# Performance work log

Measured on AMD Instinct MI355X. Metric: run time of the kernel, lower is better.

Reference implementation:

```python
import jax, jax.numpy as jnp
import numpy as np
from jax import lax

NPOINT = 1024
NSAMPLE = 32
RADIUS = 0.6
BN_EPS = 1e-5


def square_distance(src, dst):
    # src (B,S,3), dst (B,N,3) -> (B,S,N) squared distances
    d = -2.0 * jnp.einsum('bsc,bnc->bsn', src, dst)
    d = d + jnp.sum(src ** 2, -1)[:, :, None]
    d = d + jnp.sum(dst ** 2, -1)[:, None, :]
    return d


def farthest_point_sample(xyz, npoint):
    B, N, _ = xyz.shape
    bidx = jnp.arange(B)

    def step(carry, _):
        distance, farthest = carry
        centroid = xyz[bidx, farthest]                      # (B,3)
        dist = jnp.sum((xyz - centroid[:, None, :]) ** 2, -1)  # (B,N)
        distance = jnp.minimum(distance, dist)
        new_far = jnp.argmax(distance, -1)
        return (distance, new_far), farthest

    init = (jnp.full((B, N), 1e10, xyz.dtype), jnp.zeros((B,), jnp.int32))
    _, idxs = lax.scan(step, init, None, length=npoint)
    return idxs.T                                            # (B,npoint)


def ball_query(xyz, new_xyz, radius, nsample):
    B, N, _ = xyz.shape
    sqr = square_distance(new_xyz, xyz)                      # (B,S,N)
    idx = jnp.where(sqr <= radius ** 2, jnp.arange(N)[None, None, :], N)
    idx = jnp.sort(idx, axis=-1)[:, :, :nsample]             # (B,S,K)
    first = idx[:, :, :1]
    return jnp.where(idx == N, first, idx)


def gather2(points, idx):
    # points (B,N,C), idx (B,S) -> (B,S,C)
    return jax.vmap(lambda p, i: p[i])(points, idx)


def gather3(points, idx):
    # points (B,N,C), idx (B,S,K) -> (B,S,K,C)
    return jax.vmap(lambda p, i: p[i])(points, idx)


def sa_forward(xyz, features, params):
    fps_idx = lax.stop_gradient(farthest_point_sample(xyz, NPOINT))
    new_xyz = gather2(xyz, fps_idx)                          # (B,S,3)
    idx = lax.stop_gradient(ball_query(xyz, new_xyz, RADIUS, NSAMPLE))
    grouped_xyz = gather3(xyz, idx) - new_xyz[:, :, None, :] # (B,S,K,3)
    grouped_feat = gather3(features.transpose(0, 2, 1), idx) # (B,S,K,C)
    g = jnp.concatenate([grouped_xyz, grouped_feat], -1)     # (B,S,K,C+3)
    g = g.transpose(0, 3, 2, 1)                              # (B,Cin,K,S)
    for w, b, ga, be in params:
        g = jnp.einsum('oc,bcks->boks', w, g) + b[None, :, None, None]
        mu = jnp.mean(g, axis=(0, 2, 3), keepdims=True)
        var = jnp.var(g, axis=(0, 2, 3), keepdims=True)
        g = ga[None, :, None, None] * (g - mu) * lax.rsqrt(var + BN_EPS) \
            + be[None, :, None, None]
        g = jax.nn.relu(g)
    new_features = jnp.max(g, axis=2)                        # (B,Cout,S)
    return new_xyz, new_features


def setup_inputs() -> dict:
    key = jax.random.key(0)
    ks = jax.random.split(key, 8)
    B, N, C = 16, 4096, 128
    cin = C + 3
    mlp = [128, 128, 256]
    inp = {
        'xyz': jax.random.normal(ks[0], (B, N, 3), jnp.float32),
        'features': jax.random.normal(ks[1], (B, C, N), jnp.float32),
    }
    prev = cin
    for i, out in enumerate(mlp):
        inp[f'w{i}'] = jax.random.normal(ks[2 + i], (out, prev), jnp.float32) * 0.05
        inp[f'b{i}'] = jnp.zeros((out,), jnp.float32)
        inp[f'gamma{i}'] = jnp.ones((out,), jnp.float32)
        inp[f'beta{i}'] = jnp.zeros((out,), jnp.float32)
        prev = out
    return inp


def reference(xyz, features, w0, b0, gamma0, beta0, w1, b1, gamma1, beta1,
              w2, b2, gamma2, beta2):
    params = [(w0, b0, gamma0, beta0), (w1, b1, gamma1, beta1),
              (w2, b2, gamma2, beta2)]
    return sa_forward(xyz, features, params)
```

## Files before the change

kernel.cpp:

```cpp
#include <hip/hip_runtime.h>

#define B_ 16
#define N_ 4096
#define S_ 1024
#define K_ 32
#define PITCH2 136
#define PITCH1 168

typedef unsigned long long u64;
typedef short bf16x8 __attribute__((ext_vector_type(8)));
typedef unsigned short u16x8 __attribute__((ext_vector_type(8)));
typedef float f32x4 __attribute__((ext_vector_type(4)));
typedef float f32x2 __attribute__((ext_vector_type(2)));

__device__ __forceinline__ unsigned short f2bf(float f) {
  unsigned u = __float_as_uint(f);
  unsigned r = (u + 0x7FFFu + ((u >> 16) & 1u)) >> 16;
  return (unsigned short)r;
}
__device__ __forceinline__ float bf2f(unsigned short h) {
  return __uint_as_float(((unsigned)h) << 16);
}

#define DPP_MAX(v, ctrl)                                                        \
  {                                                                             \
    int _t = __builtin_amdgcn_update_dpp(__float_as_int(v), __float_as_int(v),  \
                                         ctrl, 0xf, 0xf, false);                \
    v = fmaxf(v, __int_as_float(_t));                                           \
  }

__global__ __launch_bounds__(512) void k_front(
    const float* __restrict__ xyz, float* __restrict__ new_xyz,
    const float* __restrict__ feat, unsigned short* __restrict__ featT,
    const float* __restrict__ w0, const float* __restrict__ w1,
    const float* __restrict__ w2, unsigned short* __restrict__ wbf0,
    unsigned short* __restrict__ wbf1, unsigned short* __restrict__ wbf2,
    float* __restrict__ stats) {
  __shared__ __align__(16) float smem[N_ * 4 + S_ + 64];
  int blk = blockIdx.x, t = threadIdx.x;

  if (blk < 16) {
#pragma clang fp contract(off)
#if __has_builtin(__builtin_amdgcn_s_setprio)
    __builtin_amdgcn_s_setprio(3);
#endif
    float4* pts = (float4*)smem;
    int* idxs = (int*)(smem + N_ * 4);
    u64* swk = (u64*)(smem + N_ * 4 + S_);
    int b = blk;
    const float* base = xyz + (size_t)b * N_ * 3;
    for (int i = t; i < N_; i += 512)
      pts[i] = make_float4(base[i * 3], base[i * 3 + 1], base[i * 3 + 2], 0.0f);
    if (t == 0) idxs[0] = 0;
    __syncthreads();
    f32x2 px[4], py[4], pz[4], pd[4];
    int i0 = t * 8;
    #pragma unroll
    for (int j = 0; j < 4; ++j) {
      float4 p0 = pts[i0 + 2 * j], p1 = pts[i0 + 2 * j + 1];
      px[j] = (f32x2){p0.x, p1.x};
      py[j] = (f32x2){p0.y, p1.y};
      pz[j] = (f32x2){p0.z, p1.z};
      pd[j] = (f32x2){1e10f, 1e10f};
    }
    int cur = 0;
    for (int it = 0; it < S_; ++it) {
      float4 c = pts[cur];
      f32x2 c2x = (f32x2){c.x, c.x}, c2y = (f32x2){c.y, c.y}, c2z = (f32x2){c.z, c.z};
      float bestv = -1.0f; int besti = 0;
      #pragma unroll
      for (int j = 0; j < 4; ++j) {
        f32x2 dx = px[j] - c2x;
        f32x2 dy = py[j] - c2y;
        f32x2 dz = pz[j] - c2z;
        f32x2 d = (dx * dx + dy * dy) + dz * dz;
        f32x2 dm = __builtin_elementwise_min(pd[j], d);
        pd[j] = dm;
        if (dm.x > bestv) { bestv = dm.x; besti = 2 * j; }
        if (dm.y > bestv) { bestv = dm.y; besti = 2 * j + 1; }
      }
      float v = bestv;
      DPP_MAX(v, 0x111);
      DPP_MAX(v, 0x112);
      DPP_MAX(v, 0x114);
      DPP_MAX(v, 0x118);
      DPP_MAX(v, 0x142);
      DPP_MAX(v, 0x143);
      float wmax = __int_as_float(__builtin_amdgcn_readlane(__float_as_int(v), 63));
      u64 mask = __ballot(bestv == wmax);
      int owner = __ffsll((long long)mask) - 1;
      int widx = __builtin_amdgcn_readlane(i0 + besti, owner);
      if ((t & 63) == 0)
        swk[(it & 1) * 8 + (t >> 6)] =
            ((u64)__float_as_uint(wmax) << 32) | (unsigned)(4095 - widx);
      __syncthreads();
      const u64* kk = swk + (it & 1) * 8;
      u64 k0 = kk[0];
      #pragma unroll
      for (int w = 1; w < 8; ++w) if (kk[w] > k0) k0 = kk[w];
      cur = 4095 - (int)(unsigned)(k0 & 0xFFFFFFFFull);
      if (t == 0 && it + 1 < S_) idxs[it + 1] = cur;
    }
    __syncthreads();
    for (int i = t; i < S_; i += 512) {
      float4 v = pts[idxs[i]];
      size_t o = ((size_t)b * S_ + i) * 3;
      new_xyz[o] = v.x; new_xyz[o + 1] = v.y; new_xyz[o + 2] = v.z;
    }
  } else if (blk < 32) {
    int id = (blk - 16) * 512 + t;
    const int st = 16 * 512;
    for (int i = id; i < 32768; i += st) stats[i] = 0.0f;
    for (int i = id; i < 128 * 160; i += st) {
      int n = i / 160, k = i - n * 160;
      float v = (k < 128) ? w0[n * 131 + 3 + k] : (k < 131) ? w0[n * 131 + k - 128] : 0.0f;
      wbf0[i] = f2bf(v);
    }
    for (int i = id; i < 128 * 128; i += st) wbf1[i] = f2bf(w1[i]);
    for (int i = id; i < 256 * 128; i += st) wbf2[i] = f2bf(w2[i]);
  } else {
    float (*tile)[33] = (float(*)[33])smem;
    int blk2 = blk - 32;
    int n0 = (blk2 & 127) * 32;
    int c0 = ((blk2 >> 7) & 3) * 32;
    int b = blk2 >> 9;
    int tx = t & 31, ty = t >> 5;
    #pragma unroll
    for (int j = 0; j < 32; j += 16)
      tile[ty + j][tx] = feat[((size_t)b * 128 + c0 + ty + j) * N_ + n0 + tx];
    __syncthreads();
    #pragma unroll
    for (int j = 0; j < 32; j += 16)
      featT[((size_t)b * N_ + n0 + ty + j) * 128 + c0 + tx] = f2bf(tile[tx][ty + j]);
  }
}

__global__ __launch_bounds__(256) void k_ballq(const float* __restrict__ xyz,
                                               const float* __restrict__ new_xyz,
                                               int* __restrict__ ball_idx) {
  int b = blockIdx.y;
  int s = blockIdx.x * 4 + (threadIdx.x >> 6);
  int lane = threadIdx.x & 63;
  const float* pb = xyz + (size_t)b * N_ * 3;
  size_t q = (size_t)b * S_ + s;
  float qx = new_xyz[q * 3], qy = new_xyz[q * 3 + 1], qz = new_xyz[q * 3 + 2];
  float sq = __fadd_rn(__fadd_rn(__fmul_rn(qx, qx), __fmul_rn(qy, qy)), __fmul_rn(qz, qz));
  int* out = ball_idx + q * K_;
  int total = 0;
  int first_idx = -1;
  for (int basei = 0; basei < N_; basei += 64) {
    int i = basei + lane;
    float fx = pb[i * 3], fy = pb[i * 3 + 1], fz = pb[i * 3 + 2];
    float dot = __fmul_rn(qx, fx);
    dot = __fadd_rn(dot, __fmul_rn(qy, fy));
    dot = __fadd_rn(dot, __fmul_rn(qz, fz));
    float sd = __fadd_rn(__fadd_rn(__fmul_rn(fx, fx), __fmul_rn(fy, fy)), __fmul_rn(fz, fz));
    float dist = __fadd_rn(__fadd_rn(__fmul_rn(-2.0f, dot), sq), sd);
    bool within = (dist <= 0.36f);
    u64 m = __ballot(within);
    if (first_idx < 0 && m) first_idx = basei + __ffsll((long long)m) - 1;
    if (within) {
      int pos = total + __popcll(m & ((1ull << lane) - 1ull));
      if (pos < K_) out[pos] = i;
    }
    total += (int)__popcll(m);
    if (total >= K_) break;
  }
  if (total < K_) {
    int k2 = total + lane;
    if (k2 < K_) out[k2] = first_idx;
  }
}

#define MFMA(a, b, c) __builtin_amdgcn_mfma_f32_16x16x32_bf16(a, b, c, 0, 0, 0)
#define NTILES 4096

__global__ __launch_bounds__(256) void k_layer1(
    const float* __restrict__ xyz, const float* __restrict__ new_xyz,
    const unsigned short* __restrict__ featT, const int* __restrict__ ball_idx,
    const unsigned short* __restrict__ wbf0, const float* __restrict__ b0,
    unsigned short* __restrict__ y, float* __restrict__ stats) {
  __shared__ __align__(16) unsigned short Wl[128 * PITCH1];
  __shared__ float sbias[128];
  int t = threadIdx.x;
  int w = t >> 6, L = t & 63, lm = L & 15, lg = L >> 4;
  {
    int n = t >> 1, h = t & 1;
    const uint4* wr = (const uint4*)(wbf0 + n * 160 + h * 80);
    uint4* wl = (uint4*)(Wl + n * PITCH1 + h * 80);
    #pragma unroll
    for (int i = 0; i < 10; ++i) wl[i] = wr[i];
    if (t < 128) sbias[t] = b0[t];
  }
  __syncthreads();

  for (int tile = blockIdx.x; tile < NTILES; tile += gridDim.x) {
    int bb = tile >> 8;
    int s0 = (tile & 255) * 4;
    size_t qg = (size_t)bb * S_ + s0 + w;

    int p0 = ball_idx[qg * K_ + lm];
    int p1 = ball_idx[qg * K_ + 16 + lm];
    const unsigned short* f0 = featT + ((size_t)bb * N_ + p0) * 128;
    const unsigned short* f1 = featT + ((size_t)bb * N_ + p1) * 128;
    bf16x8 a0[5], a1[5];
    #pragma unroll
    for (int kt = 0; kt < 4; ++kt) {
      a0[kt] = *(const bf16x8*)(f0 + kt * 32 + lg * 8);
      a1[kt] = *(const bf16x8*)(f1 + kt * 32 + lg * 8);
    }
    a0[4] = (bf16x8){0, 0, 0, 0, 0, 0, 0, 0};
    a1[4] = (bf16x8){0, 0, 0, 0, 0, 0, 0, 0};
    if (lg == 0) {
      float nx = new_xyz[qg * 3], ny = new_xyz[qg * 3 + 1], nz = new_xyz[qg * 3 + 2];
      const float* pp0 = xyz + ((size_t)bb * N_ + p0) * 3;
      const float* pp1 = xyz + ((size_t)bb * N_ + p1) * 3;
      a0[4][0] = (short)f2bf(pp0[0] - nx);
      a0[4][1] = (short)f2bf(pp0[1] - ny);
      a0[4][2] = (short)f2bf(pp0[2] - nz);
      a1[4][0] = (short)f2bf(pp1[0] - nx);
      a1[4][1] = (short)f2bf(pp1[1] - ny);
      a1[4][2] = (short)f2bf(pp1[2] - nz);
    }
    f32x4 acc[2][8];
    #pragma unroll
    for (int mi = 0; mi < 2; ++mi)
      #pragma unroll
      for (int nt = 0; nt < 8; ++nt) acc[mi][nt] = (f32x4){0.f, 0.f, 0.f, 0.f};
    #pragma unroll
    for (int kt = 0; kt < 5; ++kt) {
      int ko = kt * 32 + lg * 8;
      bf16x8 bv[8];
      #pragma unroll
      for (int nt = 0; nt < 8; ++nt)
        bv[nt] = *(const bf16x8*)&Wl[(nt * 16 + lm) * PITCH1 + ko];
      #pragma unroll
      for (int nt = 0; nt < 8; ++nt) {
        acc[0][nt] = MFMA(a0[kt], bv[nt], acc[0][nt]);
        acc[1][nt] = MFMA(a1[kt], bv[nt], acc[1][nt]);
      }
    }
    int slot = tile & 31;
    #pragma unroll
    for (int nt = 0; nt < 8; ++nt) {
      int col = nt * 16 + lm;
      float bo = sbias[col];
      float s1 = 0.f, s2 = 0.f;
      #pragma unroll
      for (int mi = 0; mi < 2; ++mi)
        #pragma unroll
        for (int r = 0; r < 4; ++r) {
          float yv = acc[mi][nt][r] + bo;
          s1 += yv; s2 += yv * yv;
          int ks = mi * 16 + lg * 4 + r;
          y[(qg * K_ + ks) * 128 + col] = f2bf(yv);
        }
      s1 += __shfl_xor(s1, 16); s2 += __shfl_xor(s2, 16);
      s1 += __shfl_xor(s1, 32); s2 += __shfl_xor(s2, 32);
      if (lg == 0) {
        atomicAdd(stats + ((size_t)slot * 128 + col) * 2, s1);
        atomicAdd(stats + ((size_t)slot * 128 + col) * 2 + 1, s2);
      }
    }
  }
}

__global__ __launch_bounds__(256) void k_layer2(
    unsigned short* y, const float* __restrict__ stats,
    const float* __restrict__ gamma, const float* __restrict__ beta,
    const unsigned short* __restrict__ wbf1, const float* __restrict__ b1,
    float* __restrict__ stats2) {
  __shared__ __align__(16) unsigned short Wl[128 * PITCH2];
  __shared__ __align__(16) float sa[128], sd[128];
  __shared__ float sbias[128];
  int t = threadIdx.x;
  int w = t >> 6, L = t & 63, lm = L & 15, lg = L >> 4;
  if (t < 128) {
    float s1 = 0.0f, s2 = 0.0f;
    for (int sl = 0; sl < 32; ++sl) {
      s1 += stats[((size_t)sl * 128 + t) * 2];
      s2 += stats[((size_t)sl * 128 + t) * 2 + 1];
    }
    const float inv = 1.0f / 524288.0f;
    float mu = s1 * inv;
    float var = s2 * inv - mu * mu;
    float a = gamma[t] * rsqrtf(var + 1e-5f);
    sa[t] = a;
    sd[t] = beta[t] - a * mu;
    sbias[t] = b1[t];
  }
  {
    int n = t >> 1, h = t & 1;
    const uint4* wr = (const uint4*)(wbf1 + n * 128 + h * 64);
    uint4* wl = (uint4*)(Wl + n * PITCH2 + h * 64);
    #pragma unroll
    for (int i = 0; i < 8; ++i) wl[i] = wr[i];
  }
  __syncthreads();

  for (int tile = blockIdx.x; tile < NTILES; tile += gridDim.x) {
    int bb = tile >> 8;
    int s0 = (tile & 255) * 4;
    size_t qg = (size_t)bb * S_ + s0 + w;

    const u16x8* yr0 = (const u16x8*)(y + (qg * K_ + lm) * 128);
    const u16x8* yr1 = (const u16x8*)(y + (qg * K_ + 16 + lm) * 128);
    u16x8 raw0[4], raw1[4];
    #pragma unroll
    for (int kt = 0; kt < 4; ++kt) { raw0[kt] = yr0[kt * 4 + lg]; raw1[kt] = yr1[kt * 4 + lg]; }
    bf16x8 a0[4], a1[4];
    #pragma unroll
    for (int kt = 0; kt < 4; ++kt) {
      int c = kt * 32 + lg * 8;
      f32x4 A0 = *(const f32x4*)&sa[c], A1 = *(const f32x4*)&sa[c + 4];
      f32x4 D0 = *(const f32x4*)&sd[c], D1 = *(const f32x4*)&sd[c + 4];
      #pragma unroll
      for (int j = 0; j < 4; ++j) {
        a0[kt][j]     = (short)f2bf(fmaxf(A0[j] * bf2f(raw0[kt][j])     + D0[j], 0.f));
        a0[kt][j + 4] = (short)f2bf(fmaxf(A1[j] * bf2f(raw0[kt][j + 4]) + D1[j], 0.f));
        a1[kt][j]     = (short)f2bf(fmaxf(A0[j] * bf2f(raw1[kt][j])     + D0[j], 0.f));
        a1[kt][j + 4] = (short)f2bf(fmaxf(A1[j] * bf2f(raw1[kt][j + 4]) + D1[j], 0.f));
      }
    }
    f32x4 acc[2][8];
    #pragma unroll
    for (int mi = 0; mi < 2; ++mi)
      #pragma unroll
      for (int nt = 0; nt < 8; ++nt) acc[mi][nt] = (f32x4){0.f, 0.f, 0.f, 0.f};
    #pragma unroll
    for (int kt = 0; kt < 4; ++kt) {
      int ko = kt * 32 + lg * 8;
      bf16x8 bv[8];
      #pragma unroll
      for (int nt = 0; nt < 8; ++nt)
        bv[nt] = *(const bf16x8*)&Wl[(nt * 16 + lm) * PITCH2 + ko];
      #pragma unroll
      for (int nt = 0; nt < 8; ++nt) {
        acc[0][nt] = MFMA(a0[kt], bv[nt], acc[0][nt]);
        acc[1][nt] = MFMA(a1[kt], bv[nt], acc[1][nt]);
      }
    }
    int slot = tile & 31;
    #pragma unroll
    for (int nt = 0; nt < 8; ++nt) {
      int col = nt * 16 + lm;
      float bo = sbias[col];
      float s1 = 0.f, s2 = 0.f;
      #pragma unroll
      for (int mi = 0; mi < 2; ++mi)
        #pragma unroll
        for (int r = 0; r < 4; ++r) {
          float yv = acc[mi][nt][r] + bo;
          s1 += yv; s2 += yv * yv;
          int ks = mi * 16 + lg * 4 + r;
          y[(qg * K_ + ks) * 128 + col] = f2bf(yv);
        }
      s1 += __shfl_xor(s1, 16); s2 += __shfl_xor(s2, 16);
      s1 += __shfl_xor(s1, 32); s2 += __shfl_xor(s2, 32);
      if (lg == 0) {
        atomicAdd(stats2 + ((size_t)slot * 128 + col) * 2, s1);
        atomicAdd(stats2 + ((size_t)slot * 128 + col) * 2 + 1, s2);
      }
    }
  }
}

__global__ __launch_bounds__(256) void k_layer3(
    const unsigned short* __restrict__ y, const float* __restrict__ stats2,
    const float* __restrict__ gamma, const float* __restrict__ beta,
    const unsigned short* __restrict__ wbf2, const float* __restrict__ b2,
    unsigned short* __restrict__ ymax, unsigned short* __restrict__ ymin,
    float* __restrict__ stats3) {
  __shared__ __align__(16) unsigned short Wl[128 * PITCH2];
  __shared__ __align__(16) float sa[128], sd[128];
  __shared__ float sbias[128];
  int nh = blockIdx.y, t = threadIdx.x;
  int w = t >> 6, L = t & 63, lm = L & 15, lg = L >> 4;
  if (t < 128) {
    float s1 = 0.0f, s2 = 0.0f;
    for (int sl = 0; sl < 32; ++sl) {
      s1 += stats2[((size_t)sl * 128 + t) * 2];
      s2 += stats2[((size_t)sl * 128 + t) * 2 + 1];
    }
    const float inv = 1.0f / 524288.0f;
    float mu = s1 * inv;
    float var = s2 * inv - mu * mu;
    float a = gamma[t] * rsqrtf(var + 1e-5f);
    sa[t] = a;
    sd[t] = beta[t] - a * mu;
    sbias[t] = b2[nh * 128 + t];
  }
  {
    int n = t >> 1, h = t & 1;
    const uint4* wr = (const uint4*)(wbf2 + (size_t)(nh * 128 + n) * 128 + h * 64);
    uint4* wl = (uint4*)(Wl + n * PITCH2 + h * 64);
    #pragma unroll
    for (int i = 0; i < 8; ++i) wl[i] = wr[i];
  }
  __syncthreads();

  for (int tile = blockIdx.x; tile < NTILES; tile += gridDim.x) {
    int bb = tile >> 8;
    int s0 = (tile & 255) * 4;
    size_t qg = (size_t)bb * S_ + s0 + w;

    const u16x8* yr0 = (const u16x8*)(y + (qg * K_ + lm) * 128);
    const u16x8* yr1 = (const u16x8*)(y + (qg * K_ + 16 + lm) * 128);
    u16x8 raw0[4], raw1[4];
    #pragma unroll
    for (int kt = 0; kt < 4; ++kt) { raw0[kt] = yr0[kt * 4 + lg]; raw1[kt] = yr1[kt * 4 + lg]; }
    bf16x8 a0[4], a1[4];
    #pragma unroll
    for (int kt = 0; kt < 4; ++kt) {
      int c = kt * 32 + lg * 8;
      f32x4 A0 = *(const f32x4*)&sa[c], A1 = *(const f32x4*)&sa[c + 4];
      f32x4 D0 = *(const f32x4*)&sd[c], D1 = *(const f32x4*)&sd[c + 4];
      #pragma unroll
      for (int j = 0; j < 4; ++j) {
        a0[kt][j]     = (short)f2bf(fmaxf(A0[j] * bf2f(raw0[kt][j])     + D0[j], 0.f));
        a0[kt][j + 4] = (short)f2bf(fmaxf(A1[j] * bf2f(raw0[kt][j + 4]) + D1[j], 0.f));
        a1[kt][j]     = (short)f2bf(fmaxf(A0[j] * bf2f(raw1[kt][j])     + D0[j], 0.f));
        a1[kt][j + 4] = (short)f2bf(fmaxf(A1[j] * bf2f(raw1[kt][j + 4]) + D1[j], 0.f));
      }
    }
    f32x4 acc[2][8];
    #pragma unroll
    for (int mi = 0; mi < 2; ++mi)
      #pragma unroll
      for (int nt = 0; nt < 8; ++nt) acc[mi][nt] = (f32x4){0.f, 0.f, 0.f, 0.f};
    #pragma unroll
    for (int kt = 0; kt < 4; ++kt) {
      int ko = kt * 32 + lg * 8;
      bf16x8 bv[8];
      #pragma unroll
      for (int nt = 0; nt < 8; ++nt)
        bv[nt] = *(const bf16x8*)&Wl[(nt * 16 + lm) * PITCH2 + ko];
      #pragma unroll
      for (int nt = 0; nt < 8; ++nt) {
        acc[0][nt] = MFMA(a0[kt], bv[nt], acc[0][nt]);
        acc[1][nt] = MFMA(a1[kt], bv[nt], acc[1][nt]);
      }
    }
    int slot = tile & 31;
    #pragma unroll
    for (int nt = 0; nt < 8; ++nt) {
      int col = nt * 16 + lm;
      int o = nh * 128 + col;
      float bo = sbias[col];
      float s1 = 0.f, s2 = 0.f, mx = -3.4e38f, mn = 3.4e38f;
      #pragma unroll
      for (int mi = 0; mi < 2; ++mi)
        #pragma unroll
        for (int r = 0; r < 4; ++r) {
          float yv = acc[mi][nt][r] + bo;
          s1 += yv; s2 += yv * yv;
          mx = fmaxf(mx, yv); mn = fminf(mn, yv);
        }
      s1 += __shfl_xor(s1, 16); s2 += __shfl_xor(s2, 16);
      s1 += __shfl_xor(s1, 32); s2 += __shfl_xor(s2, 32);
      mx = fmaxf(mx, __shfl_xor(mx, 16)); mx = fmaxf(mx, __shfl_xor(mx, 32));
      mn = fminf(mn, __shfl_xor(mn, 16)); mn = fminf(mn, __shfl_xor(mn, 32));
      if (lg == 0) {
        ymax[qg * 256 + o] = f2bf(mx);
        ymin[qg * 256 + o] = f2bf(mn);
        atomicAdd(stats3 + ((size_t)slot * 256 + o) * 2, s1);
        atomicAdd(stats3 + ((size_t)slot * 256 + o) * 2 + 1, s2);
      }
    }
  }
}

__global__ __launch_bounds__(256) void k_final(const unsigned short* __restrict__ ymax,
                                               const unsigned short* __restrict__ ymin,
                                               const float* __restrict__ stats3,
                                               const float* __restrict__ gamma,
                                               const float* __restrict__ beta,
                                               float* __restrict__ out2) {
  __shared__ float tile[32][33];
  __shared__ float smA[32], smD[32];
  int b = blockIdx.z, o0 = blockIdx.y * 32, s0 = blockIdx.x * 32;
  int tx = threadIdx.x, ty = threadIdx.y;
  if (ty == 0) {
    int c = o0 + tx;
    float s1 = 0.0f, s2 = 0.0f;
    for (int sl = 0; sl < 32; ++sl) {
      s1 += stats3[((size_t)sl * 256 + c) * 2];
      s2 += stats3[((size_t)sl * 256 + c) * 2 + 1];
    }
    const float inv = 1.0f / 524288.0f;
    float mu = s1 * inv;
    float var = s2 * inv - mu * mu;
    float a = gamma[c] * rsqrtf(var + 1e-5f);
    smA[tx] = a;
    smD[tx] = beta[c] - a * mu;
  }
  __syncthreads();
  float a_rd = smA[tx];
  #pragma unroll
  for (int j = 0; j < 32; j += 8) {
    size_t src = ((size_t)b * S_ + s0 + ty + j) * 256 + o0 + tx;
    tile[ty + j][tx] = (a_rd >= 0.0f) ? bf2f(ymax[src]) : bf2f(ymin[src]);
  }
  __syncthreads();
  #pragma unroll
  for (int j = 0; j < 32; j += 8) {
    float a = smA[ty + j], dd = smD[ty + j];
    out2[((size_t)b * 256 + o0 + ty + j) * S_ + s0 + tx] = fmaxf(a * tile[tx][ty + j] + dd, 0.0f);
  }
}

extern "C" void kernel_launch(void* const* d_in, const int* in_sizes, int n_in,
                              void* d_out, int out_size, void* d_ws, size_t ws_size,
                              hipStream_t stream) {
  (void)in_sizes; (void)n_in; (void)out_size; (void)ws_size;
  const float* xyz  = (const float*)d_in[0];
  const float* feat = (const float*)d_in[1];
  const float* w0   = (const float*)d_in[2];
  const float* b0   = (const float*)d_in[3];
  const float* ga0  = (const float*)d_in[4];
  const float* be0  = (const float*)d_in[5];
  const float* w1   = (const float*)d_in[6];
  const float* b1   = (const float*)d_in[7];
  const float* ga1  = (const float*)d_in[8];
  const float* be1  = (const float*)d_in[9];
  const float* w2   = (const float*)d_in[10];
  const float* b2   = (const float*)d_in[11];
  const float* ga2  = (const float*)d_in[12];
  const float* be2  = (const float*)d_in[13];

  float* out_xyz  = (float*)d_out;
  float* out_feat = out_xyz + (size_t)B_ * S_ * 3;

  char* ws = (char*)d_ws;
  size_t off = 0;
  auto alloc = [&](size_t bytes) -> void* {
    void* p = ws + off;
    off += (bytes + 255) & ~(size_t)255;
    return p;
  };
  unsigned short* featT = (unsigned short*)alloc((size_t)B_ * N_ * 128 * 2);
  int*   ball  = (int*)alloc((size_t)B_ * S_ * K_ * 4);
  float* stats = (float*)alloc(32768 * 4);
  unsigned short* wbf0 = (unsigned short*)alloc(128 * 160 * 2);
  unsigned short* wbf1 = (unsigned short*)alloc(128 * 128 * 2);
  unsigned short* wbf2 = (unsigned short*)alloc(256 * 128 * 2);
  unsigned short* ymaxb = (unsigned short*)alloc((size_t)B_ * S_ * 256 * 2);
  unsigned short* yminb = (unsigned short*)alloc((size_t)B_ * S_ * 256 * 2);
  unsigned short* y = (unsigned short*)alloc((size_t)B_ * S_ * K_ * 128 * 2);

  k_front<<<16 + 16 + 8192, 512, 0, stream>>>(xyz, out_xyz, feat, featT,
                                              w0, w1, w2, wbf0, wbf1, wbf2, stats);
  k_ballq<<<dim3(256, 16), 256, 0, stream>>>(xyz, out_xyz, ball);
  k_layer1<<<768, 256, 0, stream>>>(xyz, out_xyz, featT, ball, wbf0, b0, y, stats);
  k_layer2<<<1024, 256, 0, stream>>>(y, stats, ga0, be0, wbf1, b1, stats + 8192);
  k_layer3<<<dim3(512, 2), 256, 0, stream>>>(y, stats + 8192, ga1, be1, wbf2, b2,
                                             ymaxb, yminb, stats + 16384);
  k_final<<<dim3(32, 8, 16), dim3(32, 8), 0, stream>>>(ymaxb, yminb, stats + 16384,
                                                       ga2, be2, out_feat);
}
```

Baseline: 1.084 ms.

## Fuse ball query into FPS block with producer-consumer waves and flag sync

```diff
diff --git a/kernel.cpp b/kernel.cpp
--- a/kernel.cpp
+++ b/kernel.cpp
@@ -29,87 +29,138 @@
     v = fmaxf(v, __int_as_float(_t));                                           \
   }
 
-__global__ __launch_bounds__(512) void k_front(
+__global__ __launch_bounds__(1024) void k_front(
     const float* __restrict__ xyz, float* __restrict__ new_xyz,
     const float* __restrict__ feat, unsigned short* __restrict__ featT,
     const float* __restrict__ w0, const float* __restrict__ w1,
     const float* __restrict__ w2, unsigned short* __restrict__ wbf0,
     unsigned short* __restrict__ wbf1, unsigned short* __restrict__ wbf2,
-    float* __restrict__ stats) {
-  __shared__ __align__(16) float smem[N_ * 4 + S_ + 64];
+    float* __restrict__ stats, int* __restrict__ ball_idx) {
+  __shared__ __align__(16) float smem[16384 + 1024 + 16 + 8 + 8];
   int blk = blockIdx.x, t = threadIdx.x;
 
   if (blk < 16) {
 #pragma clang fp contract(off)
-#if __has_builtin(__builtin_amdgcn_s_setprio)
-    __builtin_amdgcn_s_setprio(3);
-#endif
     float4* pts = (float4*)smem;
-    int* idxs = (int*)(smem + N_ * 4);
-    u64* swk = (u64*)(smem + N_ * 4 + S_);
+    int* idxs = (int*)(smem + 16384);
+    u64* kslot = (u64*)(smem + 16384 + 1024);
+    unsigned* cnt = (unsigned*)(smem + 16384 + 1024 + 16);
+    unsigned* prog = (unsigned*)(smem + 16384 + 1024 + 16 + 8);
     int b = blk;
     const float* base = xyz + (size_t)b * N_ * 3;
-    for (int i = t; i < N_; i += 512)
+    for (int i = t; i < N_; i += 1024)
       pts[i] = make_float4(base[i * 3], base[i * 3 + 1], base[i * 3 + 2], 0.0f);
-    if (t == 0) idxs[0] = 0;
+    if (t < 8) cnt[t] = 0;
+    if (t == 8) *prog = 0;
     __syncthreads();
-    f32x2 px[4], py[4], pz[4], pd[4];
-    int i0 = t * 8;
-    #pragma unroll
-    for (int j = 0; j < 4; ++j) {
-      float4 p0 = pts[i0 + 2 * j], p1 = pts[i0 + 2 * j + 1];
-      px[j] = (f32x2){p0.x, p1.x};
-      py[j] = (f32x2){p0.y, p1.y};
-      pz[j] = (f32x2){p0.z, p1.z};
-      pd[j] = (f32x2){1e10f, 1e10f};
-    }
-    int cur = 0;
-    for (int it = 0; it < S_; ++it) {
-      float4 c = pts[cur];
-      f32x2 c2x = (f32x2){c.x, c.x}, c2y = (f32x2){c.y, c.y}, c2z = (f32x2){c.z, c.z};
-      float bestv = -1.0f; int besti = 0;
+
+    int wv = t >> 6, lane = t & 63;
+    if (wv < 8) {
+#if __has_builtin(__builtin_amdgcn_s_setprio)
+      __builtin_amdgcn_s_setprio(3);
+#endif
+      f32x2 px[4], py[4], pz[4], pd[4];
+      int i0 = t * 8;
       #pragma unroll
       for (int j = 0; j < 4; ++j) {
-        f32x2 dx = px[j] - c2x;
-        f32x2 dy = py[j] - c2y;
-        f32x2 dz = pz[j] - c2z;
-        f32x2 d = (dx * dx + dy * dy) + dz * dz;
-        f32x2 dm = __builtin_elementwise_min(pd[j], d);
-        pd[j] = dm;
-        if (dm.x > bestv) { bestv = dm.x; besti = 2 * j; }
-        if (dm.y > bestv) { bestv = dm.y; besti = 2 * j + 1; }
-      }
-      float v = bestv;
-      DPP_MAX(v, 0x111);
-      DPP_MAX(v, 0x112);
-      DPP_MAX(v, 0x114);
-      DPP_MAX(v, 0x118);
-      DPP_MAX(v, 0x142);
-      DPP_MAX(v, 0x143);
-      float wmax = __int_as_float(__builtin_amdgcn_readlane(__float_as_int(v), 63));
-      u64 mask = __ballot(bestv == wmax);
-      int owner = __ffsll((long long)mask) - 1;
-      int widx = __builtin_amdgcn_readlane(i0 + besti, owner);
-      if ((t & 63) == 0)
-        swk[(it & 1) * 8 + (t >> 6)] =
-            ((u64)__float_as_uint(wmax) << 32) | (unsigned)(4095 - widx);
-      __syncthreads();
-      const u64* kk = swk + (it & 1) * 8;
-      u64 k0 = kk[0];
-      #pragma unroll
-      for (int w = 1; w < 8; ++w) if (kk[w] > k0) k0 = kk[w];
-      cur = 4095 - (int)(unsigned)(k0 & 0xFFFFFFFFull);
-      if (t == 0 && it + 1 < S_) idxs[it + 1] = cur;
-    }
-    __syncthreads();
-    for (int i = t; i < S_; i += 512) {
-      float4 v = pts[idxs[i]];
-      size_t o = ((size_t)b * S_ + i) * 3;
-      new_xyz[o] = v.x; new_xyz[o + 1] = v.y; new_xyz[o + 2] = v.z;
+        float4 p0 = pts[i0 + 2 * j], p1 = pts[i0 + 2 * j + 1];
+        px[j] = (f32x2){p0.x, p1.x};
+        py[j] = (f32x2){p0.y, p1.y};
+        pz[j] = (f32x2){p0.z, p1.z};
+        pd[j] = (f32x2){1e10f, 1e10f};
+      }
+      int cur = 0;
+      for (int it = 0; it < S_; ++it) {
+        float4 c = pts[cur];
+        if (t == 0) {
+          idxs[it] = cur;
+          __hip_atomic_store(prog, (unsigned)(it + 1), __ATOMIC_RELEASE,
+                             __HIP_MEMORY_SCOPE_WORKGROUP);
+          size_t o = ((size_t)b * S_ + it) * 3;
+          new_xyz[o] = c.x; new_xyz[o + 1] = c.y; new_xyz[o + 2] = c.z;
+        }
+        f32x2 c2x = (f32x2){c.x, c.x}, c2y = (f32x2){c.y, c.y}, c2z = (f32x2){c.z, c.z};
+        float bestv = -1.0f; int besti = 0;
+        #pragma unroll
+        for (int j = 0; j < 4; ++j) {
+          f32x2 dx = px[j] - c2x;
+          f32x2 dy = py[j] - c2y;
+          f32x2 dz = pz[j] - c2z;
+          f32x2 d = (dx * dx + dy * dy) + dz * dz;
+          f32x2 dm = __builtin_elementwise_min(pd[j], d);
+          pd[j] = dm;
+          if (dm.x > bestv) { bestv = dm.x; besti = 2 * j; }
+          if (dm.y > bestv) { bestv = dm.y; besti = 2 * j + 1; }
+        }
+        float v = bestv;
+        DPP_MAX(v, 0x111);
+        DPP_MAX(v, 0x112);
+        DPP_MAX(v, 0x114);
+        DPP_MAX(v, 0x118);
+        DPP_MAX(v, 0x142);
+        DPP_MAX(v, 0x143);
+        float wmax = __int_as_float(__builtin_amdgcn_readlane(__float_as_int(v), 63));
+        u64 mask = __ballot(bestv == wmax);
+        int owner = __ffsll((long long)mask) - 1;
+        int widx = __builtin_amdgcn_readlane(i0 + besti, owner);
+        u64 mykey = ((u64)__float_as_uint(wmax) << 32) | (unsigned)(4095 - widx);
+        if (lane == 0) {
+          kslot[wv] = mykey;
+          __hip_atomic_store(&cnt[wv], (unsigned)(it + 1), __ATOMIC_RELEASE,
+                             __HIP_MEMORY_SCOPE_WORKGROUP);
+        }
+        int src = lane & 7;
+        while (__hip_atomic_load(&cnt[src], __ATOMIC_ACQUIRE,
+                                 __HIP_MEMORY_SCOPE_WORKGROUP) < (unsigned)(it + 1)) {}
+        u64 k2 = __hip_atomic_load(&kslot[src], __ATOMIC_RELAXED,
+                                   __HIP_MEMORY_SCOPE_WORKGROUP);
+        #pragma unroll
+        for (int d = 1; d < 8; d <<= 1) {
+          u64 o2 = __shfl_xor(k2, d);
+          if (o2 > k2) k2 = o2;
+        }
+        cur = 4095 - (int)(unsigned)(k2 & 0xFFFull);
+      }
+    } else {
+      int wq = wv - 8;
+      for (int s = wq; s < S_; s += 8) {
+        while (__hip_atomic_load(prog, __ATOMIC_ACQUIRE,
+                                 __HIP_MEMORY_SCOPE_WORKGROUP) < (unsigned)(s + 1)) {}
+        int ci = idxs[s];
+        float4 cq = pts[ci];
+        float qx = cq.x, qy = cq.y, qz = cq.z;
+        float sq = __fadd_rn(__fadd_rn(__fmul_rn(qx, qx), __fmul_rn(qy, qy)),
+                             __fmul_rn(qz, qz));
+        int* out = ball_idx + ((size_t)b * S_ + s) * K_;
+        int total = 0;
+        int first_idx = -1;
+        for (int basei = 0; basei < N_; basei += 64) {
+          float4 p = pts[basei + lane];
+          float dot = __fmul_rn(qx, p.x);
+          dot = __fadd_rn(dot, __fmul_rn(qy, p.y));
+          dot = __fadd_rn(dot, __fmul_rn(qz, p.z));
+          float sd = __fadd_rn(__fadd_rn(__fmul_rn(p.x, p.x), __fmul_rn(p.y, p.y)),
+                               __fmul_rn(p.z, p.z));
+          float dist = __fadd_rn(__fadd_rn(__fmul_rn(-2.0f, dot), sq), sd);
+          bool within = (dist <= 0.36f);
+          u64 m = __ballot(within);
+          if (first_idx < 0 && m) first_idx = basei + __ffsll((long long)m) - 1;
+          if (within) {
+            int pos = total + __popcll(m & ((1ull << lane) - 1ull));
+            if (pos < K_) out[pos] = basei + lane;
+          }
+          total += (int)__popcll(m);
+          if (total >= K_) break;
+        }
+        if (total < K_) {
+          int k2 = total + lane;
+          if (k2 < K_) out[k2] = first_idx;
+        }
+      }
     }
   } else if (blk < 32) {
-    int id = (blk - 16) * 512 + t;
-    const int st = 16 * 512;
+    int id = (blk - 16) * 1024 + t;
+    const int st = 16 * 1024;
     for (int i = id; i < 32768; i += st) stats[i] = 0.0f;
     for (int i = id; i < 128 * 160; i += st) {
       int n = i / 160, k = i - n * 160;
@@ -125,50 +176,9 @@
     int c0 = ((blk2 >> 7) & 3) * 32;
     int b = blk2 >> 9;
     int tx = t & 31, ty = t >> 5;
-    #pragma unroll
-    for (int j = 0; j < 32; j += 16)
-      tile[ty + j][tx] = feat[((size_t)b * 128 + c0 + ty + j) * N_ + n0 + tx];
+    tile[ty][tx] = feat[((size_t)b * 128 + c0 + ty) * N_ + n0 + tx];
     __syncthreads();
-    #pragma unroll
-    for (int j = 0; j < 32; j += 16)
-      featT[((size_t)b * N_ + n0 + ty + j) * 128 + c0 + tx] = f2bf(tile[tx][ty + j]);
-  }
-}
-
-__global__ __launch_bounds__(256) void k_ballq(const float* __restrict__ xyz,
-                                               const float* __restrict__ new_xyz,
-                                               int* __restrict__ ball_idx) {
-  int b = blockIdx.y;
-  int s = blockIdx.x * 4 + (threadIdx.x >> 6);
-  int lane = threadIdx.x & 63;
-  const float* pb = xyz + (size_t)b * N_ * 3;
-  size_t q = (size_t)b * S_ + s;
-  float qx = new_xyz[q * 3], qy = new_xyz[q * 3 + 1], qz = new_xyz[q * 3 + 2];
-  float sq = __fadd_rn(__fadd_rn(__fmul_rn(qx, qx), __fmul_rn(qy, qy)), __fmul_rn(qz, qz));
-  int* out = ball_idx + q * K_;
-  int total = 0;
-  int first_idx = -1;
-  for (int basei = 0; basei < N_; basei += 64) {
-    int i = basei + lane;
-    float fx = pb[i * 3], fy = pb[i * 3 + 1], fz = pb[i * 3 + 2];
-    float dot = __fmul_rn(qx, fx);
-    dot = __fadd_rn(dot, __fmul_rn(qy, fy));
-    dot = __fadd_rn(dot, __fmul_rn(qz, fz));
-    float sd = __fadd_rn(__fadd_rn(__fmul_rn(fx, fx), __fmul_rn(fy, fy)), __fmul_rn(fz, fz));
-    float dist = __fadd_rn(__fadd_rn(__fmul_rn(-2.0f, dot), sq), sd);
-    bool within = (dist <= 0.36f);
-    u64 m = __ballot(within);
-    if (first_idx < 0 && m) first_idx = basei + __ffsll((long long)m) - 1;
-    if (within) {
-      int pos = total + __popcll(m & ((1ull << lane) - 1ull));
-      if (pos < K_) out[pos] = i;
-    }
-    total += (int)__popcll(m);
-    if (total >= K_) break;
-  }
-  if (total < K_) {
-    int k2 = total + lane;
-    if (k2 < K_) out[k2] = first_idx;
+    featT[((size_t)b * N_ + n0 + ty) * 128 + c0 + tx] = f2bf(tile[tx][ty]);
   }
 }
 
@@ -548,9 +558,9 @@
   unsigned short* yminb = (unsigned short*)alloc((size_t)B_ * S_ * 256 * 2);
   unsigned short* y = (unsigned short*)alloc((size_t)B_ * S_ * K_ * 128 * 2);
 
-  k_front<<<16 + 16 + 8192, 512, 0, stream>>>(xyz, out_xyz, feat, featT,
-                                              w0, w1, w2, wbf0, wbf1, wbf2, stats);
-  k_ballq<<<dim3(256, 16), 256, 0, stream>>>(xyz, out_xyz, ball);
+  k_front<<<16 + 16 + 8192, 1024, 0, stream>>>(xyz, out_xyz, feat, featT,
+                                               w0, w1, w2, wbf0, wbf1, wbf2,
+                                               stats, ball);
   k_layer1<<<768, 256, 0, stream>>>(xyz, out_xyz, featT, ball, wbf0, b0, y, stats);
   k_layer2<<<1024, 256, 0, stream>>>(y, stats, ga0, be0, wbf1, b1, stats + 8192);
   k_layer3<<<dim3(512, 2), 256, 0, stream>>>(y, stats + 8192, ga1, be1, wbf2, b2,
```

New measurement: 1.684 ms. 55.3% more time.
